# Optimization experiments

Hardware: AMD Instinct MI355X
Metric: run time of the kernel (lower is better)

## Reference

```python
import jax, jax.numpy as jnp
import numpy as np

DIM = 256


def setup_inputs() -> dict:
    key = jax.random.key(0)
    ks = jax.random.split(key, 10)
    d = DIM
    inp = {
        "agent": jax.random.normal(ks[0], (64, d), dtype=jnp.float32),
        "x": jax.random.normal(ks[1], (8, 4096, d), dtype=jnp.float32),
        # parameters (stored as [in, out]; y = x @ W + b)
        "W_qkv": jax.random.normal(ks[2], (d, 3 * d), dtype=jnp.float32) * (d ** -0.5),
        "b_qkv": jnp.zeros((3 * d,), dtype=jnp.float32),
        "W_agent": jax.random.normal(ks[3], (d, 2 * d), dtype=jnp.float32) * (d ** -0.5),
        "b_agent": jnp.zeros((2 * d,), dtype=jnp.float32),
        "W_fc1": jax.random.normal(ks[4], (d, d), dtype=jnp.float32) * (d ** -0.5),
        "b_fc1": jnp.zeros((d,), dtype=jnp.float32),
        "W_fc2": jax.random.normal(ks[5], (d, d), dtype=jnp.float32) * (d ** -0.5),
        "b_fc2": jnp.zeros((d,), dtype=jnp.float32),
    }
    return inp


def reference(agent, x, W_qkv, b_qkv, W_agent, b_agent, W_fc1, b_fc1, W_fc2, b_fc2):
    d = x.shape[-1]
    scale = d ** -0.5
    # qkv projection of tokens: [B,N,3d] -> q,k,v each [B,N,d]
    qkv = x @ W_qkv + b_qkv
    q, k, v = jnp.split(qkv, 3, axis=-1)
    # agent projection: [K,2d] -> q_agent,k_agent each [K,d]
    ag = agent @ W_agent + b_agent
    q_agent, k_agent = jnp.split(ag, 2, axis=-1)
    # stage 1: agents attend over tokens -> [B,K,N]
    attn1 = jax.nn.softmax(jnp.einsum('kd,bnd->bkn', q_agent, k) * scale, axis=-1)
    va = jnp.einsum('bkn,bnd->bkd', attn1, v)  # [B,K,d]
    va = va @ W_fc1 + b_fc1
    # stage 2: tokens attend over agents -> [B,N,K]
    attn2 = jax.nn.softmax(jnp.einsum('bnd,kd->bnk', q, k_agent) * scale, axis=-1)
    out = jnp.einsum('bnk,bkd->bnd', attn2, va)  # [B,N,d]
    out = out @ W_fc2 + b_fc2
    return out + x
```

## Files before the change

kernel.cpp:

```cpp
#include <hip/hip_runtime.h>
#include <stdint.h>
#include <string.h>

#define BB 8
#define NN 4096
#define DD 256
#define SCALE 0.0625f
#define XS 264
#define XT 72

using frag_ab = __attribute__((ext_vector_type(8))) short;
using frag_cd = __attribute__((ext_vector_type(4))) float;

__device__ __forceinline__ unsigned short f2bf(float f) {
    union { float f; unsigned u; } a; a.f = f;
    unsigned r = a.u + 0x7FFFu + ((a.u >> 16) & 1u);
    return (unsigned short)(r >> 16);
}
__device__ __forceinline__ float bf2f(unsigned short h) {
    union { unsigned u; float f; } a; a.u = ((unsigned)h) << 16;
    return a.f;
}

__global__ __launch_bounds__(256) void k_setup(
    const float* __restrict__ agent, const float* __restrict__ Wag,
    const float* __restrict__ bag, const float* __restrict__ Wqkv,
    const float* __restrict__ bqkv, const float* __restrict__ Wfc1,
    const float* __restrict__ bfc1, const float* __restrict__ Wfc2,
    unsigned short* __restrict__ P12t, float* __restrict__ c2,
    unsigned short* __restrict__ W3b, float* __restrict__ b3)
{
    __shared__ float arow[256];
    __shared__ float red[4][256];
    float* redf = &red[0][0];
    const int bx = blockIdx.x, tid = threadIdx.x;
    const int w = tid >> 6, lane = tid & 63;
    if (bx < 128) {
        const int c = bx;
        const int woff = (c < 64) ? 256 : 0;
        const int aoff = (c < 64) ? 0 : 256;
        const int row = c & 63;
        {
            float p4[4] = {0.f, 0.f, 0.f, 0.f};
            for (int oo = 0; oo < 64; ++oo) {
                const int o = w * 64 + oo;
                const float ao = agent[row * 256 + o];
#pragma unroll
                for (int jj = 0; jj < 4; ++jj)
                    p4[jj] += ao * Wag[o * 512 + aoff + jj * 64 + lane];
            }
#pragma unroll
            for (int jj = 0; jj < 4; ++jj) red[w][jj * 64 + lane] = p4[jj];
        }
        __syncthreads();
        arow[tid] = bag[aoff + tid] + red[0][tid] + red[1][tid] + red[2][tid] + red[3][tid];
        __syncthreads();
        {
            const float4* wr = (const float4*)&Wqkv[(size_t)tid * 768 + woff];
            float s = 0.f;
#pragma unroll 4
            for (int o4 = 0; o4 < 64; ++o4) {
                float4 v = wr[o4];
                s += v.x * arow[o4 * 4] + v.y * arow[o4 * 4 + 1] +
                     v.z * arow[o4 * 4 + 2] + v.w * arow[o4 * 4 + 3];
            }
            P12t[(size_t)c * 256 + tid] = f2bf(SCALE * s);
        }
        if (c >= 64) {
            __syncthreads();
            redf[tid] = bqkv[woff + tid] * arow[tid];
            __syncthreads();
            for (int st = 128; st; st >>= 1) {
                if (tid < st) redf[tid] += redf[tid + st];
                __syncthreads();
            }
            if (tid == 0) c2[c - 64] = SCALE * redf[0];
        }
    } else {
        const int i = bx - 128;
        const bool isb3 = (bx == 384);
        {
            float p4[4] = {0.f, 0.f, 0.f, 0.f};
            for (int oo = 0; oo < 64; ++oo) {
                const int o = w * 64 + oo;
                const float wv = isb3 ? bqkv[512 + o] : Wqkv[(size_t)i * 768 + 512 + o];
#pragma unroll
                for (int jj = 0; jj < 4; ++jj)
                    p4[jj] += wv * Wfc1[o * 256 + jj * 64 + lane];
            }
#pragma unroll
            for (int jj = 0; jj < 4; ++jj) red[w][jj * 64 + lane] = p4[jj];
        }
        __syncthreads();
        arow[tid] = (isb3 ? bfc1[tid] : 0.f) +
                    red[0][tid] + red[1][tid] + red[2][tid] + red[3][tid];
        __syncthreads();
        {
            float p4[4] = {0.f, 0.f, 0.f, 0.f};
            for (int kk = 0; kk < 64; ++kk) {
                const int k = w * 64 + kk;
                const float av = arow[k];
#pragma unroll
                for (int jj = 0; jj < 4; ++jj)
                    p4[jj] += av * Wfc2[k * 256 + jj * 64 + lane];
            }
#pragma unroll
            for (int jj = 0; jj < 4; ++jj) red[w][jj * 64 + lane] = p4[jj];
        }
        __syncthreads();
        const float o4 = red[0][tid] + red[1][tid] + red[2][tid] + red[3][tid];
        if (isb3) b3[tid] = o4;
        else      W3b[(size_t)i * 256 + tid] = f2bf(o4);
    }
}

__global__ __launch_bounds__(256) void k_fuse(
    const float* __restrict__ x, const unsigned short* __restrict__ P12t,
    const float* __restrict__ c2, unsigned short* __restrict__ p2b,
    unsigned short* __restrict__ part, float* __restrict__ statS)
{
    __shared__ unsigned short xtile[64 * XS];
    __shared__ unsigned short Bs[128 * XT];
    __shared__ unsigned short Pl[64 * XT];
    __shared__ float Ss[4][64];
    const int s = blockIdx.x, b = blockIdx.y;
    const int n0 = s * 64;
    const int tid = threadIdx.x;
    const int w = tid >> 6, lane = tid & 63;
    const int ml = lane & 15, q = lane >> 4;

#pragma unroll
    for (int p = 0; p < 16; ++p) {
        int idx = p * 256 + tid;
        int tok = idx >> 6, d = (idx & 63) * 4;
        float4 v = *(const float4*)&x[(size_t)(b * 4096 + n0 + tok) * 256 + d];
        unsigned short u[4] = {f2bf(v.x), f2bf(v.y), f2bf(v.z), f2bf(v.w)};
        uint2 pk; memcpy(&pk, u, 8);
        *(uint2*)&xtile[tok * XS + d] = pk;
    }
    __syncthreads();

    frag_cd acc1[8];
#pragma unroll
    for (int j = 0; j < 8; ++j)
#pragma unroll
        for (int r = 0; r < 4; ++r) acc1[j][r] = 0.f;

    uint4 pre[4];
#pragma unroll
    for (int p = 0; p < 4; ++p) {
        int idx = p * 256 + tid;
        int r = idx >> 3, c = (idx & 7) * 8;
        pre[p] = *(const uint4*)&P12t[(size_t)r * 256 + c];
    }
    for (int kbi = 0; kbi < 4; ++kbi) {
        const int kb = kbi * 64;
        __syncthreads();
#pragma unroll
        for (int p = 0; p < 4; ++p) {
            int idx = p * 256 + tid;
            int r = idx >> 3, c = (idx & 7) * 8;
            *(uint4*)&Bs[r * XT + c] = pre[p];
        }
        if (kbi < 3) {
#pragma unroll
            for (int p = 0; p < 4; ++p) {
                int idx = p * 256 + tid;
                int r = idx >> 3, c = (idx & 7) * 8;
                pre[p] = *(const uint4*)&P12t[(size_t)r * 256 + kb + 64 + c];
            }
        }
        __syncthreads();
#pragma unroll
        for (int ks = 0; ks < 2; ++ks) {
            const int kk = ks * 32 + q * 8;
            frag_ab a = *(const frag_ab*)&xtile[(w * 16 + ml) * XS + kb + kk];
#pragma unroll
            for (int j = 0; j < 8; ++j) {
                frag_ab bf = *(const frag_ab*)&Bs[(j * 16 + ml) * XT + kk];
                acc1[j] = __builtin_amdgcn_mfma_f32_16x16x32_bf16(a, bf, acc1[j], 0, 0, 0);
            }
        }
    }

    {
        float cc[4];
#pragma unroll
        for (int j = 0; j < 4; ++j) cc[j] = c2[j * 16 + ml];
#pragma unroll
        for (int r = 0; r < 4; ++r) {
            float e[4], sum = 0.f;
#pragma unroll
            for (int j = 0; j < 4; ++j) {
                e[j] = __expf(acc1[4 + j][r] + cc[j]);
                sum += e[j];
            }
#pragma unroll
            for (int mask = 1; mask <= 8; mask <<= 1) sum += __shfl_xor(sum, mask);
            float inv = 1.f / sum;
            const int tok = n0 + w * 16 + q * 4 + r;
#pragma unroll
            for (int j = 0; j < 4; ++j)
                p2b[(size_t)(b * 4096 + tok) * 64 + j * 16 + ml] = f2bf(e[j] * inv);
        }
    }

    float e1[4][4];
#pragma unroll
    for (int j = 0; j < 4; ++j) {
#pragma unroll
        for (int r = 0; r < 4; ++r) e1[j][r] = __expf(acc1[j][r]);
        float sj = e1[j][0] + e1[j][1] + e1[j][2] + e1[j][3];
        sj += __shfl_xor(sj, 16);
        sj += __shfl_xor(sj, 32);
        if (lane < 16) Ss[w][j * 16 + ml] = sj;
    }

#pragma unroll
    for (int j = 0; j < 4; ++j)
#pragma unroll
        for (int r = 0; r < 4; ++r)
            Pl[(j * 16 + ml) * XT + w * 16 + q * 4 + r] = f2bf(e1[j][r]);
    __syncthreads();

    if (tid < 64)
        statS[(size_t)(b * 64 + tid) * 64 + s] =
            Ss[0][tid] + Ss[1][tid] + Ss[2][tid] + Ss[3][tid];

    frag_cd acc2[4][4];
#pragma unroll
    for (int af = 0; af < 4; ++af)
#pragma unroll
        for (int i = 0; i < 4; ++i)
#pragma unroll
            for (int r = 0; r < 4; ++r) acc2[af][i][r] = 0.f;
#pragma unroll
    for (int ks = 0; ks < 2; ++ks) {
        const int kk = ks * 32 + q * 8;
        frag_ab a[4], bf[4];
#pragma unroll
        for (int af = 0; af < 4; ++af)
            a[af] = *(const frag_ab*)&Pl[(af * 16 + ml) * XT + kk];
#pragma unroll
        for (int i = 0; i < 4; ++i) {
            const int d = w * 64 + i * 16 + ml;
            unsigned short u[8];
#pragma unroll
            for (int t = 0; t < 8; ++t) u[t] = xtile[(kk + t) * XS + d];
            memcpy(&bf[i], u, 16);
        }
#pragma unroll
        for (int af = 0; af < 4; ++af)
#pragma unroll
            for (int i = 0; i < 4; ++i)
                acc2[af][i] = __builtin_amdgcn_mfma_f32_16x16x32_bf16(
                    a[af], bf[i], acc2[af][i], 0, 0, 0);
    }
#pragma unroll
    for (int af = 0; af < 4; ++af)
#pragma unroll
        for (int i = 0; i < 4; ++i)
#pragma unroll
            for (int r = 0; r < 4; ++r)
                part[(size_t)((s * 8 + b) * 64 + af * 16 + q * 4 + r) * 256 +
                     w * 64 + i * 16 + ml] = f2bf(acc2[af][i][r]);
}

__global__ __launch_bounds__(256) void k_fc(
    const unsigned short* __restrict__ part, const float* __restrict__ statS,
    const unsigned short* __restrict__ W3b, const float* __restrict__ b3,
    unsigned short* __restrict__ va3t)
{
    __shared__ float red[4][256];
    __shared__ float rowb[256];
    __shared__ float rs[64];
    const int row = blockIdx.x, tid = threadIdx.x;
    const int b = row >> 6, agc = row & 63;
    const int w = tid >> 6, lane = tid & 63;
    {
        float p4[4] = {0.f, 0.f, 0.f, 0.f};
        for (int ss = 0; ss < 16; ++ss) {
            const int s = w * 16 + ss;
            uint2 pk = *(const uint2*)&part[(size_t)((s * 8 + b) * 64 + agc) * 256 + lane * 4];
            unsigned short u[4]; memcpy(u, &pk, 8);
#pragma unroll
            for (int k = 0; k < 4; ++k) p4[k] += bf2f(u[k]);
        }
#pragma unroll
        for (int k = 0; k < 4; ++k) red[w][lane * 4 + k] = p4[k];
    }
    if (tid < 64) rs[tid] = statS[(size_t)(b * 64 + agc) * 64 + tid];
    __syncthreads();
    float tot = 0.f;
#pragma unroll
    for (int t = 0; t < 64; ++t) tot += rs[t];
    rowb[tid] = (red[0][tid] + red[1][tid] + red[2][tid] + red[3][tid]) / tot;
    __syncthreads();
    {
        float p4[4] = {0.f, 0.f, 0.f, 0.f};
        for (int kk = 0; kk < 64; ++kk) {
            const int k = w * 64 + kk;
            const float rv = rowb[k];
#pragma unroll
            for (int jj = 0; jj < 4; ++jj)
                p4[jj] += rv * bf2f(W3b[(size_t)k * 256 + jj * 64 + lane]);
        }
#pragma unroll
        for (int jj = 0; jj < 4; ++jj) red[w][jj * 64 + lane] = p4[jj];
    }
    __syncthreads();
    const float s2 = b3[tid] + red[0][tid] + red[1][tid] + red[2][tid] + red[3][tid];
    va3t[(size_t)(b * 256 + tid) * 64 + agc] = f2bf(s2);
}

__global__ __launch_bounds__(256) void k_stage2(
    const unsigned short* __restrict__ p2b, const unsigned short* __restrict__ va3t,
    const float* __restrict__ x, const float* __restrict__ bfc2,
    float* __restrict__ out)
{
    __shared__ unsigned short Vs[256 * 72];
    __shared__ unsigned short Ps[64 * 72];
    const int n0 = blockIdx.x * 64, b = blockIdx.y;
    const int tid = threadIdx.x;
    const int w = tid >> 6, lane = tid & 63;
    const int ml = lane & 15, q = lane >> 4;

#pragma unroll
    for (int p = 0; p < 8; ++p) {
        int idx = p * 256 + tid;
        int r = idx >> 3, c = (idx & 7) * 8;
        *(uint4*)&Vs[r * 72 + c] = *(const uint4*)&va3t[(size_t)(b * 256 + r) * 64 + c];
    }
#pragma unroll
    for (int p = 0; p < 2; ++p) {
        int idx = p * 256 + tid;
        int r = idx >> 3, c = (idx & 7) * 8;
        *(uint4*)&Ps[r * 72 + c] = *(const uint4*)&p2b[(size_t)(b * 4096 + n0 + r) * 64 + c];
    }
    __syncthreads();

    frag_cd acc[4][4];
#pragma unroll
    for (int i = 0; i < 4; ++i)
#pragma unroll
        for (int j = 0; j < 4; ++j)
#pragma unroll
            for (int r = 0; r < 4; ++r) acc[i][j][r] = 0.f;
#pragma unroll
    for (int ks = 0; ks < 2; ++ks) {
        const int kk = ks * 32 + q * 8;
        frag_ab a[4], bf[4];
#pragma unroll
        for (int i = 0; i < 4; ++i)
            a[i] = *(const frag_ab*)&Vs[(w * 64 + i * 16 + ml) * 72 + kk];
#pragma unroll
        for (int j = 0; j < 4; ++j)
            bf[j] = *(const frag_ab*)&Ps[(j * 16 + ml) * 72 + kk];
#pragma unroll
        for (int i = 0; i < 4; ++i)
#pragma unroll
            for (int j = 0; j < 4; ++j)
                acc[i][j] = __builtin_amdgcn_mfma_f32_16x16x32_bf16(
                    a[i], bf[j], acc[i][j], 0, 0, 0);
    }

#pragma unroll
    for (int i = 0; i < 4; ++i) {
        const int d0 = w * 64 + i * 16 + q * 4;
        float4 bias = *(const float4*)&bfc2[d0];
#pragma unroll
        for (int j = 0; j < 4; ++j) {
            const int tok = n0 + j * 16 + ml;
            size_t ad = (size_t)(b * 4096 + tok) * 256 + d0;
            float4 xr = *(const float4*)&x[ad];
            float4 o;
            o.x = acc[i][j][0] + bias.x + xr.x;
            o.y = acc[i][j][1] + bias.y + xr.y;
            o.z = acc[i][j][2] + bias.z + xr.z;
            o.w = acc[i][j][3] + bias.w + xr.w;
            *(float4*)&out[ad] = o;
        }
    }
}

extern "C" void kernel_launch(void* const* d_in, const int* in_sizes, int n_in,
                              void* d_out, int out_size, void* d_ws, size_t ws_size,
                              hipStream_t stream) {
    const float* agent = (const float*)d_in[0];
    const float* x     = (const float*)d_in[1];
    const float* Wqkv  = (const float*)d_in[2];
    const float* bqkv  = (const float*)d_in[3];
    const float* Wag   = (const float*)d_in[4];
    const float* bag   = (const float*)d_in[5];
    const float* Wfc1  = (const float*)d_in[6];
    const float* bfc1  = (const float*)d_in[7];
    const float* Wfc2  = (const float*)d_in[8];
    const float* bfc2  = (const float*)d_in[9];
    float* out = (float*)d_out;

    char* wsp = (char*)d_ws;
    size_t off = 0;
    unsigned short* p2b  = (unsigned short*)(wsp + off); off += (size_t)BB * NN * 64 * 2;
    unsigned short* part = (unsigned short*)(wsp + off); off += (size_t)64 * BB * 64 * 256 * 2;
    float* statS = (float*)(wsp + off); off += (size_t)BB * 64 * 64 * 4;
    unsigned short* P12t = (unsigned short*)(wsp + off); off += (size_t)128 * 256 * 2;
    float* c2   = (float*)(wsp + off); off += 256 * 4;
    unsigned short* W3b = (unsigned short*)(wsp + off); off += (size_t)256 * 256 * 2;
    float* b3   = (float*)(wsp + off); off += 256 * 4;
    unsigned short* va3t = (unsigned short*)(wsp + off); off += (size_t)BB * DD * 64 * 2;

    k_setup<<<385, 256, 0, stream>>>(agent, Wag, bag, Wqkv, bqkv, Wfc1, bfc1, Wfc2,
                                     P12t, c2, W3b, b3);
    k_fuse<<<dim3(64, BB), 256, 0, stream>>>(x, P12t, c2, p2b, part, statS);
    k_fc<<<512, 256, 0, stream>>>(part, statS, W3b, b3, va3t);
    k_stage2<<<dim3(64, BB), 256, 0, stream>>>(p2b, va3t, x, bfc2, out);
}
```

Measured before the change: 180.7 us.

## Read MFMA B operands directly from global, swizzle xtile, shrink stage2 tiles

In k_fuse, the B operand (P12t) is now read straight from global/L2 into MFMA fragments instead of being staged through a shared-memory buffer with barriers. The A fragments of x are preloaded into registers, and the x tile in LDS uses an XOR swizzle to cut bank conflicts on the strided transposed reads. k_stage2 drops its LDS staging, reads va3t and p2b from global directly, and halves the token tile so it launches twice as many blocks. This removes LDS traffic and __syncthreads. The cost is uncoalesced, redundant global fragment loads and more register pressure from the preloaded fragments.

```diff
diff --git a/kernel.cpp b/kernel.cpp
--- a/kernel.cpp
+++ b/kernel.cpp
@@ -20,6 +20,10 @@
 __device__ __forceinline__ float bf2f(unsigned short h) {
     union { unsigned u; float f; } a; a.u = ((unsigned)h) << 16;
     return a.f;
+}
+__device__ __forceinline__ int xsw(int tok, int d) {
+    const int e = ((tok >> 3) & 3) << 1;
+    return tok * XS + (d & 7) + (((d >> 3) ^ e) << 3);
 }
 
 __global__ __launch_bounds__(256) void k_setup(
@@ -120,7 +124,6 @@
     unsigned short* __restrict__ part, float* __restrict__ statS)
 {
     __shared__ unsigned short xtile[64 * XS];
-    __shared__ unsigned short Bs[128 * XT];
     __shared__ unsigned short Pl[64 * XT];
     __shared__ float Ss[4][64];
     const int s = blockIdx.x, b = blockIdx.y;
@@ -136,9 +139,17 @@
         float4 v = *(const float4*)&x[(size_t)(b * 4096 + n0 + tok) * 256 + d];
         unsigned short u[4] = {f2bf(v.x), f2bf(v.y), f2bf(v.z), f2bf(v.w)};
         uint2 pk; memcpy(&pk, u, 8);
-        *(uint2*)&xtile[tok * XS + d] = pk;
-    }
-    __syncthreads();
+        *(uint2*)&xtile[xsw(tok, d)] = pk;
+    }
+    __syncthreads();
+
+    frag_ab afr[8];
+#pragma unroll
+    for (int kb4 = 0; kb4 < 4; ++kb4)
+#pragma unroll
+        for (int ks = 0; ks < 2; ++ks)
+            afr[kb4 * 2 + ks] =
+                *(const frag_ab*)&xtile[xsw(w * 16 + ml, kb4 * 64 + ks * 32 + q * 8)];
 
     frag_cd acc1[8];
 #pragma unroll
@@ -146,38 +157,14 @@
 #pragma unroll
         for (int r = 0; r < 4; ++r) acc1[j][r] = 0.f;
 
-    uint4 pre[4];
-#pragma unroll
-    for (int p = 0; p < 4; ++p) {
-        int idx = p * 256 + tid;
-        int r = idx >> 3, c = (idx & 7) * 8;
-        pre[p] = *(const uint4*)&P12t[(size_t)r * 256 + c];
-    }
-    for (int kbi = 0; kbi < 4; ++kbi) {
-        const int kb = kbi * 64;
-        __syncthreads();
-#pragma unroll
-        for (int p = 0; p < 4; ++p) {
-            int idx = p * 256 + tid;
-            int r = idx >> 3, c = (idx & 7) * 8;
-            *(uint4*)&Bs[r * XT + c] = pre[p];
-        }
-        if (kbi < 3) {
-#pragma unroll
-            for (int p = 0; p < 4; ++p) {
-                int idx = p * 256 + tid;
-                int r = idx >> 3, c = (idx & 7) * 8;
-                pre[p] = *(const uint4*)&P12t[(size_t)r * 256 + kb + 64 + c];
-            }
-        }
-        __syncthreads();
+    for (int kb4 = 0; kb4 < 4; ++kb4) {
 #pragma unroll
         for (int ks = 0; ks < 2; ++ks) {
-            const int kk = ks * 32 + q * 8;
-            frag_ab a = *(const frag_ab*)&xtile[(w * 16 + ml) * XS + kb + kk];
+            const int kk = kb4 * 64 + ks * 32 + q * 8;
+            const frag_ab a = afr[kb4 * 2 + ks];
 #pragma unroll
             for (int j = 0; j < 8; ++j) {
-                frag_ab bf = *(const frag_ab*)&Bs[(j * 16 + ml) * XT + kk];
+                frag_ab bf = *(const frag_ab*)&P12t[(size_t)(j * 16 + ml) * 256 + kk];
                 acc1[j] = __builtin_amdgcn_mfma_f32_16x16x32_bf16(a, bf, acc1[j], 0, 0, 0);
             }
         }
@@ -246,7 +233,7 @@
             const int d = w * 64 + i * 16 + ml;
             unsigned short u[8];
 #pragma unroll
-            for (int t = 0; t < 8; ++t) u[t] = xtile[(kk + t) * XS + d];
+            for (int t = 0; t < 8; ++t) u[t] = xtile[xsw(kk + t, d)];
             memcpy(&bf[i], u, 16);
         }
 #pragma unroll
@@ -318,48 +305,32 @@
     const float* __restrict__ x, const float* __restrict__ bfc2,
     float* __restrict__ out)
 {
-    __shared__ unsigned short Vs[256 * 72];
-    __shared__ unsigned short Ps[64 * 72];
-    const int n0 = blockIdx.x * 64, b = blockIdx.y;
+    const int n0 = blockIdx.x * 32, b = blockIdx.y;
     const int tid = threadIdx.x;
     const int w = tid >> 6, lane = tid & 63;
     const int ml = lane & 15, q = lane >> 4;
 
-#pragma unroll
-    for (int p = 0; p < 8; ++p) {
-        int idx = p * 256 + tid;
-        int r = idx >> 3, c = (idx & 7) * 8;
-        *(uint4*)&Vs[r * 72 + c] = *(const uint4*)&va3t[(size_t)(b * 256 + r) * 64 + c];
-    }
-#pragma unroll
-    for (int p = 0; p < 2; ++p) {
-        int idx = p * 256 + tid;
-        int r = idx >> 3, c = (idx & 7) * 8;
-        *(uint4*)&Ps[r * 72 + c] = *(const uint4*)&p2b[(size_t)(b * 4096 + n0 + r) * 64 + c];
-    }
-    __syncthreads();
-
-    frag_cd acc[4][4];
+    frag_cd acc[4][2];
 #pragma unroll
     for (int i = 0; i < 4; ++i)
 #pragma unroll
-        for (int j = 0; j < 4; ++j)
+        for (int j = 0; j < 2; ++j)
 #pragma unroll
             for (int r = 0; r < 4; ++r) acc[i][j][r] = 0.f;
 #pragma unroll
     for (int ks = 0; ks < 2; ++ks) {
         const int kk = ks * 32 + q * 8;
-        frag_ab a[4], bf[4];
+        frag_ab a[4], bf[2];
 #pragma unroll
         for (int i = 0; i < 4; ++i)
-            a[i] = *(const frag_ab*)&Vs[(w * 64 + i * 16 + ml) * 72 + kk];
-#pragma unroll
-        for (int j = 0; j < 4; ++j)
-            bf[j] = *(const frag_ab*)&Ps[(j * 16 + ml) * 72 + kk];
+            a[i] = *(const frag_ab*)&va3t[(size_t)(b * 256 + w * 64 + i * 16 + ml) * 64 + kk];
+#pragma unroll
+        for (int j = 0; j < 2; ++j)
+            bf[j] = *(const frag_ab*)&p2b[(size_t)(b * 4096 + n0 + j * 16 + ml) * 64 + kk];
 #pragma unroll
         for (int i = 0; i < 4; ++i)
 #pragma unroll
-            for (int j = 0; j < 4; ++j)
+            for (int j = 0; j < 2; ++j)
                 acc[i][j] = __builtin_amdgcn_mfma_f32_16x16x32_bf16(
                     a[i], bf[j], acc[i][j], 0, 0, 0);
     }
@@ -369,7 +340,7 @@
         const int d0 = w * 64 + i * 16 + q * 4;
         float4 bias = *(const float4*)&bfc2[d0];
 #pragma unroll
-        for (int j = 0; j < 4; ++j) {
+        for (int j = 0; j < 2; ++j) {
             const int tok = n0 + j * 16 + ml;
             size_t ad = (size_t)(b * 4096 + tok) * 256 + d0;
             float4 xr = *(const float4*)&x[ad];
@@ -413,5 +384,5 @@
                                      P12t, c2, W3b, b3);
     k_fuse<<<dim3(64, BB), 256, 0, stream>>>(x, P12t, c2, p2b, part, statS);
     k_fc<<<512, 256, 0, stream>>>(part, statS, W3b, b3, va3t);
-    k_stage2<<<dim3(64, BB), 256, 0, stream>>>(p2b, va3t, x, bfc2, out);
-}
+    k_stage2<<<dim3(128, BB), 256, 0, stream>>>(p2b, va3t, x, bfc2, out);
+}
```

Result: faster. 164.5 us (-8.9%).
